# Optimization experiments

Measured on AMD Instinct MI355X. Metric: run time of the kernel, lower is better.

The kernel has to match this reference:

```python
import jax, jax.numpy as jnp
import numpy as np

Q, B, S, D, N = 4, 8, 1024, 768, 1024
H = 2 * D // 3  # 512, from encoder hidden = 2*dim//3
TAU = 1e-6      # eval-mode gumbel temperature
BN_EPS = 1e-5


def setup_inputs() -> dict:
    key = jax.random.key(0)
    ks = jax.random.split(key, 12)
    rn = lambda k, sh, sc=0.02: (jax.random.normal(k, sh, jnp.float32) * sc)
    u = jax.random.uniform(ks[0], (Q, B, S, N), jnp.float32, 1e-9, 1.0)
    return {
        "x": jax.random.normal(ks[1], (B, S, D), jnp.float32),
        "codebooks": rn(ks[2], (Q, N, D), 0.05),
        # posterior MLPs (per-quantizer, stacked over Q): Linear+BN(eval)+ReLU x2
        "pW1": rn(ks[3], (Q, D, H)), "pb1": jnp.zeros((Q, H)),
        "pg1": jnp.ones((Q, H)), "pbe1": jnp.zeros((Q, H)),
        "pm1": jnp.zeros((Q, H)), "pv1": jnp.ones((Q, H)),
        "pW2": rn(ks[4], (Q, H, N)), "pb2": jnp.zeros((Q, N)),
        "pg2": jnp.ones((Q, N)), "pbe2": jnp.zeros((Q, N)),
        "pm2": jnp.zeros((Q, N)), "pv2": jnp.ones((Q, N)),
        # shared decoder: D -> 2D -> D
        "dW1": rn(ks[5], (D, 2 * D)), "db1": jnp.zeros((2 * D,)),
        "dg1": jnp.ones((2 * D,)), "dbe1": jnp.zeros((2 * D,)),
        "dm1": jnp.zeros((2 * D,)), "dv1": jnp.ones((2 * D,)),
        "dW2": rn(ks[6], (2 * D, D)), "db2": jnp.zeros((D,)),
        "dg2": jnp.ones((D,)), "dbe2": jnp.zeros((D,)),
        "dm2": jnp.zeros((D,)), "dv2": jnp.ones((D,)),
        # precomputed gumbel noise (deterministic replacement for F.gumbel_softmax sampling)
        "gumbel": -jnp.log(-jnp.log(u)),
    }


def _bn(x, g, b, m, v):
    # eval-mode BatchNorm1d over the last (channel) axis
    return (x - m) * (g * jax.lax.rsqrt(v + BN_EPS)) + b


def _blk(x, W, b, g, be, m, v):
    return jax.nn.relu(_bn(x @ W + b, g, be, m, v))


def reference(x, codebooks, pW1, pb1, pg1, pbe1, pm1, pv1,
              pW2, pb2, pg2, pbe2, pm2, pv2,
              dW1, db1, dg1, dbe1, dm1, dv1,
              dW2, db2, dg2, dbe2, dm2, dv2, gumbel):
    residual = x
    quantized_out = jnp.zeros_like(x)
    indices, latent_losses, entropies, zs = [], [], [], []
    for i in range(Q):
        h = _blk(residual, pW1[i], pb1[i], pg1[i], pbe1[i], pm1[i], pv1[i])
        z = _blk(h, pW2[i], pb2[i], pg2[i], pbe2[i], pm2[i], pv2[i])  # [B,S,N]
        qy = jax.nn.softmax(z, axis=2)
        entropy = -jnp.sum(qy * jnp.log(qy + 1e-10), axis=-1)          # [B,S]
        latent = qy * jnp.log(qy * N + 1e-10)                           # [B,S,N]
        # gumbel-softmax, hard=True (straight-through)
        logits = (z + gumbel[i]) / TAU
        y_soft = jax.nn.softmax(logits, axis=2)
        idx = jnp.argmax(logits, axis=2)                                # [B,S]
        y_hard = jax.nn.one_hot(idx, N, dtype=z.dtype)
        one_hot = y_hard + y_soft - jax.lax.stop_gradient(y_soft)
        z_q = jnp.einsum('bsn,nd->bsd', one_hot, codebooks[i])
        residual = residual - jax.lax.stop_gradient(z_q)
        quantized_out = quantized_out + z_q
        indices.append(idx); latent_losses.append(latent)
        zs.append(z); entropies.append(entropy)
    h = _blk(quantized_out, dW1, db1, dg1, dbe1, dm1, dv1)
    xhat = _blk(h, dW2, db2, dg2, dbe2, dm2, dv2)
    return (xhat,
            jnp.stack(entropies, axis=0),
            jnp.stack(latent_losses, axis=0),
            jnp.stack(indices, axis=0),
            jnp.stack(zs, axis=0))
```

## Files before the change

### kernel.cpp

```cpp
#include <hip/hip_runtime.h>

namespace {

constexpr int QN = 4;
constexpr int MR = 8192;
constexpr int DD = 768;
constexpr int HH = 512;
constexpr int NN = 1024;
constexpr float DELTA = 0.008f;

typedef __attribute__((ext_vector_type(8))) __bf16 bf16x8;
typedef __attribute__((ext_vector_type(4))) __bf16 bf16x4;
typedef __attribute__((ext_vector_type(4))) float  f32x4;

#define GL2LDS(g, l) __builtin_amdgcn_global_load_lds( \
    (const __attribute__((address_space(1))) void*)(g), \
    (__attribute__((address_space(3))) void*)(l), 16, 0, 0)

__global__ void zcnt(int* __restrict__ cnt)
{
    if (threadIdx.x < QN) cnt[threadIdx.x] = 0;
}

__global__ __launch_bounds__(256)
void wcvt(const float* __restrict__ src, __bf16* __restrict__ dst, int K, int N)
{
    __shared__ float tile[32][33];
    const size_t bo = (size_t)blockIdx.z * K * N;
    const int n0 = blockIdx.x * 32, k0 = blockIdx.y * 32;
    const int tx = threadIdx.x, ty = threadIdx.y;
    #pragma unroll
    for (int i = 0; i < 4; ++i)
        tile[ty + 8 * i][tx] = src[bo + (size_t)(k0 + ty + 8 * i) * N + n0 + tx];
    __syncthreads();
    #pragma unroll
    for (int i = 0; i < 4; ++i)
        dst[bo + (size_t)(n0 + ty + 8 * i) * K + k0 + tx] = (__bf16)tile[tx][ty + 8 * i];
}

__global__ __launch_bounds__(256)
void acvt(const float* __restrict__ src, __bf16* __restrict__ dst)
{
    const size_t i = ((size_t)blockIdx.x * 256 + threadIdx.x) * 8;
    float4 a = *(const float4*)(src + i);
    float4 b = *(const float4*)(src + i + 4);
    bf16x8 o;
    o[0] = (__bf16)a.x; o[1] = (__bf16)a.y; o[2] = (__bf16)a.z; o[3] = (__bf16)a.w;
    o[4] = (__bf16)b.x; o[5] = (__bf16)b.y; o[6] = (__bf16)b.z; o[7] = (__bf16)b.w;
    *(bf16x8*)(dst + i) = o;
}

template<int OUTBF>
__global__ __launch_bounds__(256)
void gemm_mfma(const __bf16* __restrict__ A, const __bf16* __restrict__ BT,
               const float* __restrict__ bias, const float* __restrict__ gam,
               const float* __restrict__ beta, const float* __restrict__ mean,
               const float* __restrict__ var,
               float* __restrict__ C32, __bf16* __restrict__ Cbf,
               int N_, int K_)
{
    __shared__ __bf16 smem[8192];
    __bf16* As = smem;
    __bf16* Bs = smem + 4096;

    const int t   = threadIdx.x;
    const int bn0 = blockIdx.x * 128;
    const int bm0 = blockIdx.y * 128;
    const int l    = t & 63, w = t >> 6;
    const int lm   = l & 15, quad = l >> 4;
    const int mrow = (w & 1) * 64, ncol = (w >> 1) * 64;

    const int sA0 = t, sA1 = t + 256;
    const int mA0 = sA0 >> 2, qA0 = ((sA0 & 3) - (mA0 >> 1)) & 3;
    const int mA1 = sA1 >> 2, qA1 = ((sA1 & 3) - (mA1 >> 1)) & 3;
    const size_t gA0 = (size_t)(bm0 + mA0) * K_ + qA0 * 8;
    const size_t gA1 = (size_t)(bm0 + mA1) * K_ + qA1 * 8;
    const size_t gB0 = (size_t)(bn0 + mA0) * K_ + qA0 * 8;
    const size_t gB1 = (size_t)(bn0 + mA1) * K_ + qA1 * 8;

    f32x4 acc[4][4] = {};

    int aslot[4], bslot[4];
    #pragma unroll
    for (int i = 0; i < 4; ++i) {
        int m = mrow + i * 16 + lm;
        aslot[i] = m * 4 + ((quad + (m >> 1)) & 3);
        int n = ncol + i * 16 + lm;
        bslot[i] = n * 4 + ((quad + (n >> 1)) & 3);
    }

    for (int k0 = 0; k0 < K_; k0 += 32) {
        GL2LDS(A  + gA0 + k0, As + sA0 * 8);
        GL2LDS(A  + gA1 + k0, As + sA1 * 8);
        GL2LDS(BT + gB0 + k0, Bs + sA0 * 8);
        GL2LDS(BT + gB1 + k0, Bs + sA1 * 8);
        asm volatile("s_waitcnt vmcnt(0)" ::: "memory");
        __syncthreads();

        bf16x8 af[4], bfv[4];
        #pragma unroll
        for (int i = 0; i < 4; ++i) {
            af[i]  = *(const bf16x8*)(As + aslot[i] * 8);
            bfv[i] = *(const bf16x8*)(Bs + bslot[i] * 8);
        }
        #pragma unroll
        for (int mt = 0; mt < 4; ++mt)
            #pragma unroll
            for (int nt = 0; nt < 4; ++nt)
                acc[mt][nt] = __builtin_amdgcn_mfma_f32_16x16x32_bf16(
                    af[mt], bfv[nt], acc[mt][nt], 0, 0, 0);
        __syncthreads();
    }

    float sc[4], sh[4]; int cn[4];
    #pragma unroll
    for (int nt = 0; nt < 4; ++nt) {
        int c = bn0 + ncol + nt * 16 + lm;
        cn[nt] = c;
        float s = gam[c] * rsqrtf(var[c] + 1e-5f);
        sc[nt] = s;
        sh[nt] = (bias[c] - mean[c]) * s + beta[c];
    }
    #pragma unroll
    for (int mt = 0; mt < 4; ++mt) {
        int r0 = bm0 + mrow + mt * 16 + quad * 4;
        #pragma unroll
        for (int nt = 0; nt < 4; ++nt) {
            #pragma unroll
            for (int reg = 0; reg < 4; ++reg) {
                float v = fmaxf(0.f, fmaf(acc[mt][nt][reg], sc[nt], sh[nt]));
                size_t off = (size_t)(r0 + reg) * N_ + cn[nt];
                if (OUTBF) Cbf[off] = (__bf16)v;
                else       C32[off] = v;
            }
        }
    }
}

__global__ __launch_bounds__(256)
void row_stats(const float* __restrict__ z, const float* __restrict__ gum,
               float* __restrict__ ent, float* __restrict__ lat,
               float* __restrict__ idxf, int* __restrict__ idxi,
               int* __restrict__ wl, int* __restrict__ cnt)
{
    __shared__ float sred[8];
    __shared__ int   sredi[4];
    __shared__ float stop1;
    __shared__ int   stop1i;

    const int r   = blockIdx.x;
    const int t   = threadIdx.x;
    const int wid = t >> 6;
    const bool l0 = (t & 63) == 0;

    const float4 z4 = ((const float4*)(z   + (size_t)r * NN))[t];
    const float4 g4 = ((const float4*)(gum + (size_t)r * NN))[t];

    float mx = fmaxf(fmaxf(z4.x, z4.y), fmaxf(z4.z, z4.w));
    #pragma unroll
    for (int o = 1; o < 64; o <<= 1) mx = fmaxf(mx, __shfl_xor(mx, o, 64));
    if (l0) sred[wid] = mx;
    __syncthreads();
    mx = fmaxf(fmaxf(sred[0], sred[1]), fmaxf(sred[2], sred[3]));

    float e0 = __expf(z4.x - mx), e1 = __expf(z4.y - mx);
    float e2 = __expf(z4.z - mx), e3 = __expf(z4.w - mx);
    float s = (e0 + e1) + (e2 + e3);
    #pragma unroll
    for (int o = 1; o < 64; o <<= 1) s += __shfl_xor(s, o, 64);
    if (l0) sred[4 + wid] = s;
    __syncthreads();
    s = (sred[4] + sred[5]) + (sred[6] + sred[7]);

    const float inv = 1.0f / s;
    const float q0 = e0 * inv, q1 = e1 * inv, q2 = e2 * inv, q3 = e3 * inv;

    float ep = q0 * __logf(q0 + 1e-10f) + q1 * __logf(q1 + 1e-10f)
             + q2 * __logf(q2 + 1e-10f) + q3 * __logf(q3 + 1e-10f);
    #pragma unroll
    for (int o = 1; o < 64; o <<= 1) ep += __shfl_xor(ep, o, 64);

    float4 l4;
    l4.x = q0 * __logf(q0 * 1024.f + 1e-10f);
    l4.y = q1 * __logf(q1 * 1024.f + 1e-10f);
    l4.z = q2 * __logf(q2 * 1024.f + 1e-10f);
    l4.w = q3 * __logf(q3 * 1024.f + 1e-10f);
    ((float4*)(lat + (size_t)r * NN))[t] = l4;

    const float y0 = z4.x + g4.x, y1 = z4.y + g4.y;
    const float y2 = z4.z + g4.z, y3 = z4.w + g4.w;
    float bv = y0; int bi = t * 4;
    if (y1 > bv) { bv = y1; bi = t * 4 + 1; }
    if (y2 > bv) { bv = y2; bi = t * 4 + 2; }
    if (y3 > bv) { bv = y3; bi = t * 4 + 3; }
    #pragma unroll
    for (int o = 1; o < 64; o <<= 1) {
        float ov = __shfl_xor(bv, o, 64);
        int   oi = __shfl_xor(bi, o, 64);
        if (ov > bv || (ov == bv && oi < bi)) { bv = ov; bi = oi; }
    }
    __syncthreads();
    if (l0) { sred[wid] = ep; sred[4 + wid] = bv; sredi[wid] = bi; }
    __syncthreads();
    if (t == 0) {
        ent[r] = -((sred[0] + sred[1]) + (sred[2] + sred[3]));
        float bbv = sred[4]; int bbi = sredi[0];
        #pragma unroll
        for (int ww = 1; ww < 4; ++ww)
            if (sred[4 + ww] > bbv || (sred[4 + ww] == bbv && sredi[ww] < bbi)) {
                bbv = sred[4 + ww]; bbi = sredi[ww];
            }
        stop1 = bbv; stop1i = bbi;
    }
    __syncthreads();
    const float t1v = stop1;
    const int   t1i = stop1i;

    float ex = -1e30f;
    if (t * 4 + 0 != t1i) ex = y0;
    if (t * 4 + 1 != t1i) ex = fmaxf(ex, y1);
    if (t * 4 + 2 != t1i) ex = fmaxf(ex, y2);
    if (t * 4 + 3 != t1i) ex = fmaxf(ex, y3);
    #pragma unroll
    for (int o = 1; o < 64; o <<= 1) ex = fmaxf(ex, __shfl_xor(ex, o, 64));
    __syncthreads();
    if (l0) sred[wid] = ex;
    __syncthreads();
    if (t == 0) {
        idxf[r] = (float)t1i;
        idxi[r] = t1i;
        float t2 = fmaxf(fmaxf(sred[0], sred[1]), fmaxf(sred[2], sred[3]));
        if (t1v - t2 < DELTA) {
            int p = atomicAdd(cnt, 1);
            wl[p] = r;
        }
    }
}

__global__ __launch_bounds__(256)
void recheck(const int* __restrict__ wl, const int* __restrict__ cnt,
             const float* __restrict__ gum, const float* __restrict__ Ain,
             const float* __restrict__ W1, const float* __restrict__ b1,
             const float* __restrict__ g1, const float* __restrict__ be1,
             const float* __restrict__ m1, const float* __restrict__ v1,
             const float* __restrict__ W2, const float* __restrict__ b2,
             const float* __restrict__ g2, const float* __restrict__ be2,
             const float* __restrict__ m2, const float* __restrict__ v2,
             float* __restrict__ idxf, int* __restrict__ idxi)
{
    __shared__ float rowbuf[DD];
    __shared__ float hs[HH];
    __shared__ float sred[4];
    __shared__ int   sredi[4];

    const int t   = threadIdx.x;
    const int wid = t >> 6;
    const bool l0 = (t & 63) == 0;
    const int n = cnt[0];

    for (int w = blockIdx.x; w < n; w += gridDim.x) {
        const int r = wl[w];
        __syncthreads();
        if (t < 192)
            *(float4*)&rowbuf[t * 4] = *(const float4*)(Ain + (size_t)r * DD + t * 4);
        __syncthreads();

        #pragma unroll
        for (int jj = 0; jj < 2; ++jj) {
            const int j = t + jj * 256;
            float a0 = 0.f, a1 = 0.f, a2 = 0.f, a3 = 0.f;
            #pragma unroll 4
            for (int k = 0; k < DD; k += 4) {
                a0 = fmaf(rowbuf[k + 0], W1[(size_t)(k + 0) * HH + j], a0);
                a1 = fmaf(rowbuf[k + 1], W1[(size_t)(k + 1) * HH + j], a1);
                a2 = fmaf(rowbuf[k + 2], W1[(size_t)(k + 2) * HH + j], a2);
                a3 = fmaf(rowbuf[k + 3], W1[(size_t)(k + 3) * HH + j], a3);
            }
            float a = (a0 + a1) + (a2 + a3) + b1[j];
            float scl = g1[j] * rsqrtf(v1[j] + 1e-5f);
            hs[j] = fmaxf(0.f, (a - m1[j]) * scl + be1[j]);
        }
        __syncthreads();

        float bv = -1e30f; int bi = 0;
        #pragma unroll
        for (int cc = 0; cc < 4; ++cc) {
            const int c = t + cc * 256;
            float a0 = 0.f, a1 = 0.f, a2 = 0.f, a3 = 0.f;
            #pragma unroll 4
            for (int j = 0; j < HH; j += 4) {
                a0 = fmaf(hs[j + 0], W2[(size_t)(j + 0) * NN + c], a0);
                a1 = fmaf(hs[j + 1], W2[(size_t)(j + 1) * NN + c], a1);
                a2 = fmaf(hs[j + 2], W2[(size_t)(j + 2) * NN + c], a2);
                a3 = fmaf(hs[j + 3], W2[(size_t)(j + 3) * NN + c], a3);
            }
            float a = (a0 + a1) + (a2 + a3) + b2[c];
            float scl = g2[c] * rsqrtf(v2[c] + 1e-5f);
            float zc  = fmaxf(0.f, (a - m2[c]) * scl + be2[c]);
            float y   = zc + gum[(size_t)r * NN + c];
            if (y > bv || (y == bv && c < bi)) { bv = y; bi = c; }
        }
        #pragma unroll
        for (int o = 1; o < 64; o <<= 1) {
            float ov = __shfl_xor(bv, o, 64);
            int   oi = __shfl_xor(bi, o, 64);
            if (ov > bv || (ov == bv && oi < bi)) { bv = ov; bi = oi; }
        }
        if (l0) { sred[wid] = bv; sredi[wid] = bi; }
        __syncthreads();
        if (t == 0) {
            float bbv = sred[0]; int bbi = sredi[0];
            #pragma unroll
            for (int ww = 1; ww < 4; ++ww)
                if (sred[ww] > bbv || (sred[ww] == bbv && sredi[ww] < bbi)) {
                    bbv = sred[ww]; bbi = sredi[ww];
                }
            idxf[r] = (float)bbi;
            idxi[r] = bbi;
        }
    }
}

__global__ __launch_bounds__(192)
void gather(const int* __restrict__ idxi, const float* __restrict__ cb,
            const float* __restrict__ Ain,
            float* __restrict__ res, float* __restrict__ qout,
            __bf16* __restrict__ res_bf, __bf16* __restrict__ qo_bf,
            int first, int last)
{
    const int r = blockIdx.x;
    const int t = threadIdx.x;
    const int ci = idxi[r];

    float4 c4 = *(const float4*)(cb + (size_t)ci * DD + t * 4);
    float4 rv, qv;
    if (first) {
        float4 xv = *(const float4*)(Ain + (size_t)r * DD + t * 4);
        rv.x = xv.x - c4.x; rv.y = xv.y - c4.y;
        rv.z = xv.z - c4.z; rv.w = xv.w - c4.w;
        qv = c4;
    } else {
        rv = *(const float4*)(res  + (size_t)r * DD + t * 4);
        qv = *(const float4*)(qout + (size_t)r * DD + t * 4);
        rv.x -= c4.x; rv.y -= c4.y; rv.z -= c4.z; rv.w -= c4.w;
        qv.x += c4.x; qv.y += c4.y; qv.z += c4.z; qv.w += c4.w;
    }
    *(float4*)(qout + (size_t)r * DD + t * 4) = qv;
    if (!last) {
        *(float4*)(res + (size_t)r * DD + t * 4) = rv;
        bf16x4 rb;
        rb[0] = (__bf16)rv.x; rb[1] = (__bf16)rv.y;
        rb[2] = (__bf16)rv.z; rb[3] = (__bf16)rv.w;
        *(bf16x4*)(res_bf + (size_t)r * DD + t * 4) = rb;
    } else {
        bf16x4 qb;
        qb[0] = (__bf16)qv.x; qb[1] = (__bf16)qv.y;
        qb[2] = (__bf16)qv.z; qb[3] = (__bf16)qv.w;
        *(bf16x4*)(qo_bf + (size_t)r * DD + t * 4) = qb;
    }
}

}

extern "C" void kernel_launch(void* const* d_in, const int* in_sizes, int n_in,
                              void* d_out, int out_size, void* d_ws, size_t ws_size,
                              hipStream_t stream)
{
    const float* x    = (const float*)d_in[0];
    const float* cb   = (const float*)d_in[1];
    const float* pW1  = (const float*)d_in[2];
    const float* pb1  = (const float*)d_in[3];
    const float* pg1  = (const float*)d_in[4];
    const float* pbe1 = (const float*)d_in[5];
    const float* pm1  = (const float*)d_in[6];
    const float* pv1  = (const float*)d_in[7];
    const float* pW2  = (const float*)d_in[8];
    const float* pb2  = (const float*)d_in[9];
    const float* pg2  = (const float*)d_in[10];
    const float* pbe2 = (const float*)d_in[11];
    const float* pm2  = (const float*)d_in[12];
    const float* pv2  = (const float*)d_in[13];
    const float* dW1  = (const float*)d_in[14];
    const float* db1  = (const float*)d_in[15];
    const float* dg1  = (const float*)d_in[16];
    const float* dbe1 = (const float*)d_in[17];
    const float* dm1  = (const float*)d_in[18];
    const float* dv1  = (const float*)d_in[19];
    const float* dW2  = (const float*)d_in[20];
    const float* db2  = (const float*)d_in[21];
    const float* dg2  = (const float*)d_in[22];
    const float* dbe2 = (const float*)d_in[23];
    const float* dm2  = (const float*)d_in[24];
    const float* dv2  = (const float*)d_in[25];
    const float* gum  = (const float*)d_in[26];

    float* out  = (float*)d_out;
    float* xhat = out;
    float* ent  = xhat + (size_t)MR * DD;
    float* lat  = ent  + (size_t)QN * MR;
    float* idxf = lat  + (size_t)QN * MR * NN;
    float* zs   = idxf + (size_t)QN * MR;

    char* wp = (char*)d_ws;
    float*  res   = (float*)wp;                 wp += (size_t)MR * DD * 4;
    float*  qo    = (float*)wp;                 wp += (size_t)MR * DD * 4;
    __bf16* Abf   = (__bf16*)wp;                wp += (size_t)MR * DD * 2;
    __bf16* hbf   = (__bf16*)wp;                wp += (size_t)MR * HH * 2;
    __bf16* qobf  = (__bf16*)wp;                wp += (size_t)MR * DD * 2;
    __bf16* h1bf  = (__bf16*)wp;                wp += (size_t)MR * 2 * DD * 2;
    __bf16* w1t   = (__bf16*)wp;                wp += (size_t)QN * DD * HH * 2;
    __bf16* w2t   = (__bf16*)wp;                wp += (size_t)QN * HH * NN * 2;
    __bf16* dw1t  = (__bf16*)wp;                wp += (size_t)DD * 2 * DD * 2;
    __bf16* dw2t  = (__bf16*)wp;                wp += (size_t)2 * DD * DD * 2;
    int*    idxi  = (int*)wp;                   wp += (size_t)QN * MR * 4;
    int*    wl    = (int*)wp;                   wp += (size_t)QN * MR * 4;
    int*    cnt   = (int*)wp;                   wp += 64;

    dim3 b256(256), bwc(32, 8);

    hipLaunchKernelGGL(zcnt, dim3(1), dim3(64), 0, stream, cnt);
    hipLaunchKernelGGL(wcvt, dim3(HH / 32, DD / 32, QN), bwc, 0, stream, pW1, w1t, DD, HH);
    hipLaunchKernelGGL(wcvt, dim3(NN / 32, HH / 32, QN), bwc, 0, stream, pW2, w2t, HH, NN);
    hipLaunchKernelGGL(wcvt, dim3(2 * DD / 32, DD / 32, 1), bwc, 0, stream, dW1, dw1t, DD, 2 * DD);
    hipLaunchKernelGGL(wcvt, dim3(DD / 32, 2 * DD / 32, 1), bwc, 0, stream, dW2, dw2t, 2 * DD, DD);
    hipLaunchKernelGGL(acvt, dim3((size_t)MR * DD / (8 * 256)), b256, 0, stream, x, Abf);

    for (int i = 0; i < QN; ++i) {
        hipLaunchKernelGGL((gemm_mfma<1>), dim3(HH / 128, MR / 128), b256, 0, stream,
            Abf, w1t + (size_t)i * DD * HH,
            pb1 + i * HH, pg1 + i * HH, pbe1 + i * HH, pm1 + i * HH, pv1 + i * HH,
            (float*)nullptr, hbf, HH, DD);
        float* z_i = zs + (size_t)i * MR * NN;
        hipLaunchKernelGGL((gemm_mfma<0>), dim3(NN / 128, MR / 128), b256, 0, stream,
            hbf, w2t + (size_t)i * HH * NN,
            pb2 + i * NN, pg2 + i * NN, pbe2 + i * NN, pm2 + i * NN, pv2 + i * NN,
            z_i, (__bf16*)nullptr, NN, HH);

        hipLaunchKernelGGL(row_stats, dim3(MR), b256, 0, stream,
            z_i, gum + (size_t)i * MR * NN,
            ent + (size_t)i * MR, lat + (size_t)i * MR * NN, idxf + (size_t)i * MR,
            idxi + (size_t)i * MR, wl + (size_t)i * MR, cnt + i);

        const float* Ain = (i == 0) ? x : res;
        hipLaunchKernelGGL(recheck, dim3(256), b256, 0, stream,
            wl + (size_t)i * MR, cnt + i, gum + (size_t)i * MR * NN, Ain,
            pW1 + (size_t)i * DD * HH, pb1 + i * HH, pg1 + i * HH, pbe1 + i * HH,
            pm1 + i * HH, pv1 + i * HH,
            pW2 + (size_t)i * HH * NN, pb2 + i * NN, pg2 + i * NN, pbe2 + i * NN,
            pm2 + i * NN, pv2 + i * NN,
            idxf + (size_t)i * MR, idxi + (size_t)i * MR);

        hipLaunchKernelGGL(gather, dim3(MR), dim3(192), 0, stream,
            idxi + (size_t)i * MR, cb + (size_t)i * NN * DD, Ain,
            res, qo, Abf, qobf, (int)(i == 0), (int)(i == QN - 1));
    }
    hipLaunchKernelGGL((gemm_mfma<1>), dim3(2 * DD / 128, MR / 128), b256, 0, stream,
        qobf, dw1t, db1, dg1, dbe1, dm1, dv1, (float*)nullptr, h1bf, 2 * DD, DD);
    hipLaunchKernelGGL((gemm_mfma<0>), dim3(DD / 128, MR / 128), b256, 0, stream,
        h1bf, dw2t, db2, dg2, dbe2, dm2, dv2, xhat, (__bf16*)nullptr, DD, 2 * DD);
}
```

Baseline: 1.306 ms.

## Triple-buffer GEMM LDS loads and fuse codebook gather into row_stats/recheck

The GEMM main loop moves from a single LDS buffer with two barriers per k-step to a three-stage ring. Global-to-LDS loads for step k+2 are issued while step k is computed, which hides load latency at the cost of three times the shared memory. The separate gather kernel is removed: rows that are confidently decided do their residual/quantized update inside row_stats, and ambiguous rows do it inside recheck from the row buffer. The zero-counter kernel is folded into acvt. This cuts launches and the idx round-trip through memory, but row_stats blocks now also carry the gather traffic.

```diff
diff --git a/kernel.cpp b/kernel.cpp
--- a/kernel.cpp
+++ b/kernel.cpp
@@ -16,11 +16,6 @@
 #define GL2LDS(g, l) __builtin_amdgcn_global_load_lds( \
     (const __attribute__((address_space(1))) void*)(g), \
     (__attribute__((address_space(3))) void*)(l), 16, 0, 0)
-
-__global__ void zcnt(int* __restrict__ cnt)
-{
-    if (threadIdx.x < QN) cnt[threadIdx.x] = 0;
-}
 
 __global__ __launch_bounds__(256)
 void wcvt(const float* __restrict__ src, __bf16* __restrict__ dst, int K, int N)
@@ -39,8 +34,10 @@
 }
 
 __global__ __launch_bounds__(256)
-void acvt(const float* __restrict__ src, __bf16* __restrict__ dst)
+void acvt(const float* __restrict__ src, __bf16* __restrict__ dst,
+          int* __restrict__ cnt)
 {
+    if (blockIdx.x == 0 && threadIdx.x < QN) cnt[threadIdx.x] = 0;
     const size_t i = ((size_t)blockIdx.x * 256 + threadIdx.x) * 8;
     float4 a = *(const float4*)(src + i);
     float4 b = *(const float4*)(src + i + 4);
@@ -59,9 +56,7 @@
                float* __restrict__ C32, __bf16* __restrict__ Cbf,
                int N_, int K_)
 {
-    __shared__ __bf16 smem[8192];
-    __bf16* As = smem;
-    __bf16* Bs = smem + 4096;
+    __shared__ __bf16 smem[24576];
 
     const int t   = threadIdx.x;
     const int bn0 = blockIdx.x * 128;
@@ -89,14 +84,43 @@
         bslot[i] = n * 4 + ((quad + (n >> 1)) & 3);
     }
 
-    for (int k0 = 0; k0 < K_; k0 += 32) {
-        GL2LDS(A  + gA0 + k0, As + sA0 * 8);
-        GL2LDS(A  + gA1 + k0, As + sA1 * 8);
-        GL2LDS(BT + gB0 + k0, Bs + sA0 * 8);
-        GL2LDS(BT + gB1 + k0, Bs + sA1 * 8);
-        asm volatile("s_waitcnt vmcnt(0)" ::: "memory");
-        __syncthreads();
-
+    const int nk = K_ >> 5;
+
+    {
+        __bf16* As = smem;
+        __bf16* Bs = smem + 4096;
+        GL2LDS(A  + gA0, As + sA0 * 8);
+        GL2LDS(A  + gA1, As + sA1 * 8);
+        GL2LDS(BT + gB0, Bs + sA0 * 8);
+        GL2LDS(BT + gB1, Bs + sA1 * 8);
+        As = smem + 8192;
+        Bs = As + 4096;
+        GL2LDS(A  + gA0 + 32, As + sA0 * 8);
+        GL2LDS(A  + gA1 + 32, As + sA1 * 8);
+        GL2LDS(BT + gB0 + 32, Bs + sA0 * 8);
+        GL2LDS(BT + gB1 + 32, Bs + sA1 * 8);
+    }
+
+    int bc = 0;
+    for (int ks = 0; ks < nk; ++ks) {
+        if (ks + 1 < nk) asm volatile("s_waitcnt vmcnt(4)" ::: "memory");
+        else             asm volatile("s_waitcnt vmcnt(0)" ::: "memory");
+        __builtin_amdgcn_s_barrier();
+        asm volatile("" ::: "memory");
+
+        if (ks + 2 < nk) {
+            int sb = bc + 2; if (sb >= 3) sb -= 3;
+            __bf16* Asn = smem + sb * 8192;
+            __bf16* Bsn = Asn + 4096;
+            const size_t ko = (size_t)(ks + 2) * 32;
+            GL2LDS(A  + gA0 + ko, Asn + sA0 * 8);
+            GL2LDS(A  + gA1 + ko, Asn + sA1 * 8);
+            GL2LDS(BT + gB0 + ko, Bsn + sA0 * 8);
+            GL2LDS(BT + gB1 + ko, Bsn + sA1 * 8);
+        }
+
+        const __bf16* As = smem + bc * 8192;
+        const __bf16* Bs = As + 4096;
         bf16x8 af[4], bfv[4];
         #pragma unroll
         for (int i = 0; i < 4; ++i) {
@@ -109,7 +133,9 @@
             for (int nt = 0; nt < 4; ++nt)
                 acc[mt][nt] = __builtin_amdgcn_mfma_f32_16x16x32_bf16(
                     af[mt], bfv[nt], acc[mt][nt], 0, 0, 0);
-        __syncthreads();
+
+        asm volatile("s_waitcnt lgkmcnt(0)" ::: "memory");
+        bc = (bc == 2) ? 0 : bc + 1;
     }
 
     float sc[4], sh[4]; int cn[4];
@@ -140,13 +166,18 @@
 __global__ __launch_bounds__(256)
 void row_stats(const float* __restrict__ z, const float* __restrict__ gum,
                float* __restrict__ ent, float* __restrict__ lat,
-               float* __restrict__ idxf, int* __restrict__ idxi,
-               int* __restrict__ wl, int* __restrict__ cnt)
+               float* __restrict__ idxf,
+               int* __restrict__ wl, int* __restrict__ cnt,
+               const float* __restrict__ Ain, const float* __restrict__ cb,
+               float* __restrict__ res, float* __restrict__ qout,
+               __bf16* __restrict__ res_bf, __bf16* __restrict__ qo_bf,
+               int first, int last)
 {
     __shared__ float sred[8];
     __shared__ int   sredi[4];
     __shared__ float stop1;
     __shared__ int   stop1i;
+    __shared__ int   sflag;
 
     const int r   = blockIdx.x;
     const int t   = threadIdx.x;
@@ -228,11 +259,36 @@
     __syncthreads();
     if (t == 0) {
         idxf[r] = (float)t1i;
-        idxi[r] = t1i;
         float t2 = fmaxf(fmaxf(sred[0], sred[1]), fmaxf(sred[2], sred[3]));
-        if (t1v - t2 < DELTA) {
-            int p = atomicAdd(cnt, 1);
-            wl[p] = r;
+        int fl = (t1v - t2 < DELTA) ? 1 : 0;
+        sflag = fl;
+        if (fl) { int p = atomicAdd(cnt, 1); wl[p] = r; }
+    }
+    __syncthreads();
+
+    if (!sflag && t < 192) {
+        float4 c4 = *(const float4*)(cb + (size_t)t1i * DD + t * 4);
+        float4 xv = *(const float4*)(Ain + (size_t)r * DD + t * 4);
+        float4 rv, qv;
+        rv.x = xv.x - c4.x; rv.y = xv.y - c4.y;
+        rv.z = xv.z - c4.z; rv.w = xv.w - c4.w;
+        if (first) { qv = c4; }
+        else {
+            qv = *(const float4*)(qout + (size_t)r * DD + t * 4);
+            qv.x += c4.x; qv.y += c4.y; qv.z += c4.z; qv.w += c4.w;
+        }
+        if (!last) {
+            *(float4*)(res  + (size_t)r * DD + t * 4) = rv;
+            *(float4*)(qout + (size_t)r * DD + t * 4) = qv;
+            bf16x4 rb;
+            rb[0] = (__bf16)rv.x; rb[1] = (__bf16)rv.y;
+            rb[2] = (__bf16)rv.z; rb[3] = (__bf16)rv.w;
+            *(bf16x4*)(res_bf + (size_t)r * DD + t * 4) = rb;
+        } else {
+            bf16x4 qb;
+            qb[0] = (__bf16)qv.x; qb[1] = (__bf16)qv.y;
+            qb[2] = (__bf16)qv.z; qb[3] = (__bf16)qv.w;
+            *(bf16x4*)(qo_bf + (size_t)r * DD + t * 4) = qb;
         }
     }
 }
@@ -246,7 +302,11 @@
              const float* __restrict__ W2, const float* __restrict__ b2,
              const float* __restrict__ g2, const float* __restrict__ be2,
              const float* __restrict__ m2, const float* __restrict__ v2,
-             float* __restrict__ idxf, int* __restrict__ idxi)
+             float* __restrict__ idxf,
+             const float* __restrict__ cb,
+             float* __restrict__ res, float* __restrict__ qout,
+             __bf16* __restrict__ res_bf, __bf16* __restrict__ qo_bf,
+             int first, int last)
 {
     __shared__ float rowbuf[DD];
     __shared__ float hs[HH];
@@ -316,47 +376,36 @@
                     bbv = sred[ww]; bbi = sredi[ww];
                 }
             idxf[r] = (float)bbi;
-            idxi[r] = bbi;
-        }
-    }
-}
-
-__global__ __launch_bounds__(192)
-void gather(const int* __restrict__ idxi, const float* __restrict__ cb,
-            const float* __restrict__ Ain,
-            float* __restrict__ res, float* __restrict__ qout,
-            __bf16* __restrict__ res_bf, __bf16* __restrict__ qo_bf,
-            int first, int last)
-{
-    const int r = blockIdx.x;
-    const int t = threadIdx.x;
-    const int ci = idxi[r];
-
-    float4 c4 = *(const float4*)(cb + (size_t)ci * DD + t * 4);
-    float4 rv, qv;
-    if (first) {
-        float4 xv = *(const float4*)(Ain + (size_t)r * DD + t * 4);
-        rv.x = xv.x - c4.x; rv.y = xv.y - c4.y;
-        rv.z = xv.z - c4.z; rv.w = xv.w - c4.w;
-        qv = c4;
-    } else {
-        rv = *(const float4*)(res  + (size_t)r * DD + t * 4);
-        qv = *(const float4*)(qout + (size_t)r * DD + t * 4);
-        rv.x -= c4.x; rv.y -= c4.y; rv.z -= c4.z; rv.w -= c4.w;
-        qv.x += c4.x; qv.y += c4.y; qv.z += c4.z; qv.w += c4.w;
-    }
-    *(float4*)(qout + (size_t)r * DD + t * 4) = qv;
-    if (!last) {
-        *(float4*)(res + (size_t)r * DD + t * 4) = rv;
-        bf16x4 rb;
-        rb[0] = (__bf16)rv.x; rb[1] = (__bf16)rv.y;
-        rb[2] = (__bf16)rv.z; rb[3] = (__bf16)rv.w;
-        *(bf16x4*)(res_bf + (size_t)r * DD + t * 4) = rb;
-    } else {
-        bf16x4 qb;
-        qb[0] = (__bf16)qv.x; qb[1] = (__bf16)qv.y;
-        qb[2] = (__bf16)qv.z; qb[3] = (__bf16)qv.w;
-        *(bf16x4*)(qo_bf + (size_t)r * DD + t * 4) = qb;
+            sredi[0] = bbi;
+        }
+        __syncthreads();
+
+        const int ci = sredi[0];
+        if (t < 192) {
+            float4 c4 = *(const float4*)(cb + (size_t)ci * DD + t * 4);
+            float4 xv = *(const float4*)&rowbuf[t * 4];
+            float4 rv, qv;
+            rv.x = xv.x - c4.x; rv.y = xv.y - c4.y;
+            rv.z = xv.z - c4.z; rv.w = xv.w - c4.w;
+            if (first) { qv = c4; }
+            else {
+                qv = *(const float4*)(qout + (size_t)r * DD + t * 4);
+                qv.x += c4.x; qv.y += c4.y; qv.z += c4.z; qv.w += c4.w;
+            }
+            if (!last) {
+                *(float4*)(res  + (size_t)r * DD + t * 4) = rv;
+                *(float4*)(qout + (size_t)r * DD + t * 4) = qv;
+                bf16x4 rb;
+                rb[0] = (__bf16)rv.x; rb[1] = (__bf16)rv.y;
+                rb[2] = (__bf16)rv.z; rb[3] = (__bf16)rv.w;
+                *(bf16x4*)(res_bf + (size_t)r * DD + t * 4) = rb;
+            } else {
+                bf16x4 qb;
+                qb[0] = (__bf16)qv.x; qb[1] = (__bf16)qv.y;
+                qb[2] = (__bf16)qv.z; qb[3] = (__bf16)qv.w;
+                *(bf16x4*)(qo_bf + (size_t)r * DD + t * 4) = qb;
+            }
+        }
     }
 }
 
@@ -412,20 +461,19 @@
     __bf16* w2t   = (__bf16*)wp;                wp += (size_t)QN * HH * NN * 2;
     __bf16* dw1t  = (__bf16*)wp;                wp += (size_t)DD * 2 * DD * 2;
     __bf16* dw2t  = (__bf16*)wp;                wp += (size_t)2 * DD * DD * 2;
-    int*    idxi  = (int*)wp;                   wp += (size_t)QN * MR * 4;
     int*    wl    = (int*)wp;                   wp += (size_t)QN * MR * 4;
     int*    cnt   = (int*)wp;                   wp += 64;
 
     dim3 b256(256), bwc(32, 8);
 
-    hipLaunchKernelGGL(zcnt, dim3(1), dim3(64), 0, stream, cnt);
     hipLaunchKernelGGL(wcvt, dim3(HH / 32, DD / 32, QN), bwc, 0, stream, pW1, w1t, DD, HH);
     hipLaunchKernelGGL(wcvt, dim3(NN / 32, HH / 32, QN), bwc, 0, stream, pW2, w2t, HH, NN);
     hipLaunchKernelGGL(wcvt, dim3(2 * DD / 32, DD / 32, 1), bwc, 0, stream, dW1, dw1t, DD, 2 * DD);
     hipLaunchKernelGGL(wcvt, dim3(DD / 32, 2 * DD / 32, 1), bwc, 0, stream, dW2, dw2t, 2 * DD, DD);
-    hipLaunchKernelGGL(acvt, dim3((size_t)MR * DD / (8 * 256)), b256, 0, stream, x, Abf);
+    hipLaunchKernelGGL(acvt, dim3((size_t)MR * DD / (8 * 256)), b256, 0, stream, x, Abf, cnt);
 
     for (int i = 0; i < QN; ++i) {
+        const int first = (i == 0), last = (i == QN - 1);
         hipLaunchKernelGGL((gemm_mfma<1>), dim3(HH / 128, MR / 128), b256, 0, stream,
             Abf, w1t + (size_t)i * DD * HH,
             pb1 + i * HH, pg1 + i * HH, pbe1 + i * HH, pm1 + i * HH, pv1 + i * HH,
@@ -436,23 +484,21 @@
             pb2 + i * NN, pg2 + i * NN, pbe2 + i * NN, pm2 + i * NN, pv2 + i * NN,
             z_i, (__bf16*)nullptr, NN, HH);
 
+        const float* Ain = (i == 0) ? x : res;
         hipLaunchKernelGGL(row_stats, dim3(MR), b256, 0, stream,
             z_i, gum + (size_t)i * MR * NN,
             ent + (size_t)i * MR, lat + (size_t)i * MR * NN, idxf + (size_t)i * MR,
-            idxi + (size_t)i * MR, wl + (size_t)i * MR, cnt + i);
-
-        const float* Ain = (i == 0) ? x : res;
+            wl + (size_t)i * MR, cnt + i,
+            Ain, cb + (size_t)i * NN * DD, res, qo, Abf, qobf, first, last);
+
         hipLaunchKernelGGL(recheck, dim3(256), b256, 0, stream,
             wl + (size_t)i * MR, cnt + i, gum + (size_t)i * MR * NN, Ain,
             pW1 + (size_t)i * DD * HH, pb1 + i * HH, pg1 + i * HH, pbe1 + i * HH,
             pm1 + i * HH, pv1 + i * HH,
             pW2 + (size_t)i * HH * NN, pb2 + i * NN, pg2 + i * NN, pbe2 + i * NN,
             pm2 + i * NN, pv2 + i * NN,
-            idxf + (size_t)i * MR, idxi + (size_t)i * MR);
-
-        hipLaunchKernelGGL(gather, dim3(MR), dim3(192), 0, stream,
-            idxi + (size_t)i * MR, cb + (size_t)i * NN * DD, Ain,
-            res, qo, Abf, qobf, (int)(i == 0), (int)(i == QN - 1));
+            idxf + (size_t)i * MR,
+            cb + (size_t)i * NN * DD, res, qo, Abf, qobf, first, last);
     }
     hipLaunchKernelGGL((gemm_mfma<1>), dim3(2 * DD / 128, MR / 128), b256, 0, stream,
         qobf, dw1t, db1, dg1, dbe1, dm1, dv1, (float*)nullptr, h1bf, 2 * DD, DD);
```

New measurement: 1.207 ms. 7.5% less time.
